# Performance work log

Hardware: AMD Instinct MI355X
Metric: run time of the kernel (lower is better)

Reference implementation:

```python
import jax, jax.numpy as jnp
import numpy as np

NUM_HEADS = 8
BN_EPS = 1e-3


def _conv2d(x, w, padding):
    # x: (B, Cin, H, W), w: (Cout, Cin, kh, kw)
    return jax.lax.conv_general_dilated(
        x, w, window_strides=(1, 1), padding=padding,
        dimension_numbers=("NCHW", "OIHW", "NCHW"))


def setup_inputs() -> dict:
    key = jax.random.key(0)
    ks = jax.random.split(key, 6)
    B, C, H, W = 8, 256, 64, 64
    L, D = 80, 256
    return {
        "img_feat": jax.random.normal(ks[0], (B, C, H, W), jnp.float32),
        "text_feats": jax.random.normal(ks[1], (B, L, D), jnp.float32),
        "proj_w": jax.random.normal(ks[2], (D, C, 1, 1), jnp.float32) * (1.0 / np.sqrt(C)),
        "proj_b": jax.random.normal(ks[3], (D,), jnp.float32) * 0.02,
        "attn_bias": jnp.zeros((NUM_HEADS,), jnp.float32),
        "scale": jnp.ones((1, NUM_HEADS, 1, 1), jnp.float32),
        "conv_w": jax.random.normal(ks[4], (C, C, 3, 3), jnp.float32) * (1.0 / np.sqrt(9 * C)),
        "bn_gamma": jnp.ones((C,), jnp.float32),
        "bn_beta": jnp.zeros((C,), jnp.float32),
        "bn_mean": jnp.zeros((C,), jnp.float32),
        "bn_var": jnp.ones((C,), jnp.float32),
    }


def reference(img_feat, text_feats, proj_w, proj_b, attn_bias, scale,
              conv_w, bn_gamma, bn_beta, bn_mean, bn_var):
    B, C, H, W = img_feat.shape
    hc = proj_w.shape[0] // NUM_HEADS  # head_channels

    # img_proj: 1x1 conv + bias -> (B, heads, hc, H, W)
    i_feat = _conv2d(img_feat, proj_w, "VALID") + proj_b[None, :, None, None]
    i_feat = i_feat.reshape(B, NUM_HEADS, hc, H, W)

    # text: (B, L, heads, hc)
    t_feat = text_feats.reshape(B, -1, NUM_HEADS, hc)

    # attn score over text tokens, then max over tokens
    attn = jnp.einsum("bmchw,bnmc->bmhwn", i_feat, t_feat)  # (B, heads, H, W, L)
    attn = jnp.max(attn, axis=-1)
    attn = attn / jnp.sqrt(jnp.asarray(hc, img_feat.dtype))
    attn = attn + attn_bias[None, :, None, None]
    attn = jax.nn.sigmoid(attn) * scale  # (B, heads, H, W)

    # project_conv: 3x3 conv (no bias) + BN (inference), no activation
    x = _conv2d(img_feat, conv_w, [(1, 1), (1, 1)])
    inv = bn_gamma / jnp.sqrt(bn_var + BN_EPS)
    x = x * inv[None, :, None, None] + (bn_beta - bn_mean * inv)[None, :, None, None]

    # gate per head and flatten back to (B, C, H, W)
    x = x.reshape(B, NUM_HEADS, -1, H, W) * attn[:, :, None]
    return x.reshape(B, -1, H, W)
```

## Files before the change

### kernel.cpp

```cpp
#include <hip/hip_runtime.h>
#include <cmath>

constexpr int kB  = 8;
constexpr int kC  = 256;
constexpr int kH  = 64;
constexpr int kW  = 64;
constexpr int kP  = kH * kW;
constexpr int kL  = 80;
constexpr int kD  = 256;
constexpr int kNH = 8;

typedef short  short8 __attribute__((ext_vector_type(8)));
typedef float  f32x4  __attribute__((ext_vector_type(4)));
typedef unsigned short ushort_t;

__device__ __forceinline__ ushort_t f2bf(float f) {
  unsigned u = __builtin_bit_cast(unsigned, f);
  u += 0x7fffu + ((u >> 16) & 1u);
  return (ushort_t)(u >> 16);
}

__device__ __forceinline__ short8 pack8(float4 a, float4 b) {
  ushort_t tmp[8] = {f2bf(a.x), f2bf(a.y), f2bf(a.z), f2bf(a.w),
                     f2bf(b.x), f2bf(b.y), f2bf(b.z), f2bf(b.w)};
  return *(short8*)tmp;
}

__global__ __launch_bounds__(256) void transpose_img_kernel(
    const float* __restrict__ img, ushort_t* __restrict__ imgT) {
  __shared__ float Ls[64 * 67];
  const int b   = blockIdx.x;
  const int p0  = blockIdx.y * 64;
  const int ci0 = blockIdx.z * 64;
  const int t   = threadIdx.x;

  for (int e = t; e < 4096; e += 256) {
    int ci = e >> 6, px = e & 63;
    Ls[px * 67 + ci] = img[((size_t)(b * kC + ci0 + ci)) * kP + p0 + px];
  }
  __syncthreads();
  for (int u = t; u < 512; u += 256) {
    int px = u >> 3, cq = (u & 7) * 8;
    ushort_t tmp[8];
#pragma unroll
    for (int j = 0; j < 8; j++) tmp[j] = f2bf(Ls[px * 67 + cq + j]);
    *(uint4*)&imgT[((size_t)(b * kP + p0 + px)) * kC + ci0 + cq] = *(uint4*)tmp;
  }
}

__global__ __launch_bounds__(256) void transpose_w2_kernel(
    const float* __restrict__ cw, ushort_t* __restrict__ w2) {
  int idx = blockIdx.x * 256 + threadIdx.x;
  if (idx >= 9 * kC * kC) return;
  int ci  = idx & 255;
  int co  = (idx >> 8) & 255;
  int tap = idx >> 16;
  w2[idx] = f2bf(cw[(co * kC + ci) * 9 + tap]);
}

__global__ __launch_bounds__(256) void attn_mfma_kernel(
    const ushort_t* __restrict__ imgT,
    const float* __restrict__ text,
    const float* __restrict__ pw,
    const float* __restrict__ pb,
    const float* __restrict__ bias,
    const float* __restrict__ scale,
    float* __restrict__ attn_out) {
  __shared__ ushort_t SI[64 * 264];

  const int b    = blockIdx.x;
  const int p0   = blockIdx.y * 64;
  const int t    = threadIdx.x;
  const int w    = t >> 6;
  const int lane = t & 63;
  const int lr   = lane & 15;
  const int lq   = lane >> 4;
  const int d0   = w * 64;

  const ushort_t* imgTb = imgT + (size_t)b * kP * kC;

  f32x4 acc[4][4] = {};

  for (int kc = 0; kc < kC; kc += 32) {
    short8 afr[4], bfr[4];
#pragma unroll
    for (int mt = 0; mt < 4; mt++) {
      const float* p = pw + (size_t)(d0 + mt * 16 + lr) * kC + kc + lq * 8;
      afr[mt] = pack8(*(const float4*)p, *(const float4*)(p + 4));
    }
#pragma unroll
    for (int nt = 0; nt < 4; nt++)
      bfr[nt] = *(const short8*)&imgTb[(size_t)(p0 + nt * 16 + lr) * kC + kc + lq * 8];
#pragma unroll
    for (int mt = 0; mt < 4; mt++)
#pragma unroll
      for (int nt = 0; nt < 4; nt++)
        acc[mt][nt] = __builtin_amdgcn_mfma_f32_16x16x32_bf16(afr[mt], bfr[nt], acc[mt][nt], 0, 0, 0);
  }

#pragma unroll
  for (int mt = 0; mt < 4; mt++) {
    float4 pb4 = *(const float4*)(pb + d0 + mt * 16 + lq * 4);
#pragma unroll
    for (int nt = 0; nt < 4; nt++) {
      ushort_t v[4];
      v[0] = f2bf(acc[mt][nt][0] + pb4.x);
      v[1] = f2bf(acc[mt][nt][1] + pb4.y);
      v[2] = f2bf(acc[mt][nt][2] + pb4.z);
      v[3] = f2bf(acc[mt][nt][3] + pb4.w);
      *(ulonglong1*)&SI[(nt * 16 + lr) * 264 + d0 + mt * 16 + lq * 4] = *(ulonglong1*)v;
    }
  }

  const float* textb = text + (size_t)b * kL * kD;
#pragma unroll
  for (int lh = 0; lh < 2; lh++) {
    const int h = 2 * w + lh;
    const float bh = bias[h], sh = scale[h];
    short8 atok[5];
#pragma unroll
    for (int mt = 0; mt < 5; mt++) {
      const float* p = textb + (size_t)(mt * 16 + lr) * kD + h * 32 + lq * 8;
      atok[mt] = pack8(*(const float4*)p, *(const float4*)(p + 4));
    }
#pragma unroll
    for (int nt = 0; nt < 4; nt++) {
      short8 bfr2 = *(const short8*)&SI[(nt * 16 + lr) * 264 + h * 32 + lq * 8];
      float vmax = -3.4e38f;
#pragma unroll
      for (int mt = 0; mt < 5; mt++) {
        f32x4 z = {};
        f32x4 d = __builtin_amdgcn_mfma_f32_16x16x32_bf16(atok[mt], bfr2, z, 0, 0, 0);
        vmax = fmaxf(vmax, fmaxf(fmaxf(d[0], d[1]), fmaxf(d[2], d[3])));
      }
      vmax = fmaxf(vmax, __shfl_xor(vmax, 16));
      vmax = fmaxf(vmax, __shfl_xor(vmax, 32));
      if (lq == 0) {
        float lg = vmax * 0.17677669529663687f + bh;
        float a  = sh / (1.0f + expf(-lg));
        attn_out[((size_t)(b * kNH + h)) * kP + p0 + nt * 16 + lr] = a;
      }
    }
  }
}

__global__ __launch_bounds__(256) void conv_mfma_kernel(
    const ushort_t* __restrict__ imgT,
    const ushort_t* __restrict__ w2,
    const float* __restrict__ gamma,
    const float* __restrict__ beta,
    const float* __restrict__ mean,
    const float* __restrict__ var,
    const float* __restrict__ attn,
    float* __restrict__ out) {
  __shared__ ushort_t Al[6 * 66 * 40];
  __shared__ ushort_t Wl[9 * 64 * 40];

  const int b   = blockIdx.x;
  const int h0  = blockIdx.y * 4;
  const int co0 = blockIdx.z * 64;
  const int t   = threadIdx.x;
  const int w   = t >> 6;
  const int lane = t & 63;
  const int lr  = lane & 15;
  const int lq  = lane >> 4;

  const ushort_t* imgTb = imgT + (size_t)b * kP * kC;

  f32x4 acc[4][4] = {};

  for (int kc = 0; kc < kC; kc += 32) {
    __syncthreads();
    for (int e = t; e < 6 * 66 * 4; e += 256) {
      int r   = e / 264;
      int rem = e - r * 264;
      int c   = rem >> 2;
      int cq  = (rem & 3) * 8;
      int row = h0 - 1 + r;
      uint4 v = make_uint4(0, 0, 0, 0);
      if (row >= 0 && row < kH && c >= 1 && c <= 64) {
        int px = row * kW + (c - 1);
        v = *(const uint4*)&imgTb[(size_t)px * kC + kc + cq];
      }
      *(uint4*)&Al[(r * 66 + c) * 40 + cq] = v;
    }
    {
      int e = t;
#pragma unroll
      for (int i = 0; i < 9; i++, e += 256) {
        int cq  = (e & 3) * 8;
        int co  = (e >> 2) & 63;
        int tap = e >> 8;
        uint4 v = *(const uint4*)&w2[((size_t)(tap * kC + co0 + co)) * kC + kc + cq];
        *(uint4*)&Wl[(tap * 64 + co) * 40 + cq] = v;
      }
    }
    __syncthreads();

    const int abase = (w * 66 + lr) * 40 + lq * 8;
    const int wbase = lr * 40 + lq * 8;
#pragma unroll
    for (int tap = 0; tap < 9; tap++) {
      const int kh = tap / 3, kw = tap % 3;
      short8 bi[4];
#pragma unroll
      for (int nt = 0; nt < 4; nt++)
        bi[nt] = *(const short8*)&Al[abase + (kh * 66 + kw + nt * 16) * 40];
      short8 aw[4];
#pragma unroll
      for (int mt = 0; mt < 4; mt++)
        aw[mt] = *(const short8*)&Wl[wbase + (tap * 64 + mt * 16) * 40];
#pragma unroll
      for (int mt = 0; mt < 4; mt++)
#pragma unroll
        for (int nt = 0; nt < 4; nt++)
          acc[mt][nt] = __builtin_amdgcn_mfma_f32_16x16x32_bf16(
              aw[mt], bi[nt], acc[mt][nt], 0, 0, 0);
    }
  }

  const int h = h0 + w;
  float* outb = out + (size_t)b * kC * kP + h * kW;
#pragma unroll
  for (int mt = 0; mt < 4; mt++) {
    const int head = (co0 + mt * 16) >> 5;
    const float* arow = attn + ((size_t)(b * kNH + head)) * kP + h * kW;
    float inv_v[4], bb_v[4];
#pragma unroll
    for (int reg = 0; reg < 4; reg++) {
      int co = co0 + mt * 16 + lq * 4 + reg;
      float inv = gamma[co] * rsqrtf(var[co] + 1e-3f);
      inv_v[reg] = inv;
      bb_v[reg]  = beta[co] - mean[co] * inv;
    }
#pragma unroll
    for (int nt = 0; nt < 4; nt++) {
      const int col = nt * 16 + lr;
      const float av = arow[col];
#pragma unroll
      for (int reg = 0; reg < 4; reg++) {
        int co = co0 + mt * 16 + lq * 4 + reg;
        outb[(size_t)co * kP + col] = (acc[mt][nt][reg] * inv_v[reg] + bb_v[reg]) * av;
      }
    }
  }
}

extern "C" void kernel_launch(void* const* d_in, const int* in_sizes, int n_in,
                              void* d_out, int out_size, void* d_ws, size_t ws_size,
                              hipStream_t stream) {
  const float* img   = (const float*)d_in[0];
  const float* text  = (const float*)d_in[1];
  const float* pw    = (const float*)d_in[2];
  const float* pb    = (const float*)d_in[3];
  const float* bias  = (const float*)d_in[4];
  const float* scale = (const float*)d_in[5];
  const float* cw    = (const float*)d_in[6];
  const float* gam   = (const float*)d_in[7];
  const float* bet   = (const float*)d_in[8];
  const float* mea   = (const float*)d_in[9];
  const float* va    = (const float*)d_in[10];
  float* out = (float*)d_out;

  char* ws = (char*)d_ws;
  float*    attn = (float*)ws;
  ushort_t* imgT = (ushort_t*)(ws + (1u << 20));
  ushort_t* w2   = (ushort_t*)(ws + (1u << 20) + (16u << 20));

  {
    dim3 grid(kB, kP / 64, kC / 64);
    transpose_img_kernel<<<grid, 256, 0, stream>>>(img, imgT);
  }
  transpose_w2_kernel<<<(9 * kC * kC + 255) / 256, 256, 0, stream>>>(cw, w2);

  {
    dim3 grid(kB, kP / 64);
    attn_mfma_kernel<<<grid, 256, 0, stream>>>(imgT, text, pw, pb, bias, scale, attn);
  }

  {
    dim3 grid(kB, kH / 4, kC / 64);
    conv_mfma_kernel<<<grid, 256, 0, stream>>>(imgT, w2, gam, bet, mea, va, attn, out);
  }
}
```

Measured before the change: 182.4 us.

## Load conv input fragments directly from global memory instead of LDS staging

The conv kernel no longer stages the image halo tile in shared memory. Each lane now reads its bf16 input fragments straight from global memory, with boundary clamping and zeroing at the edges, and skips rows that fall outside the image. The grid is reordered so the four output-channel blocks that share an input tile launch next to each other and can hit in cache, and a min-blocks-per-CU launch bound of 3 is added. This removes LDS footprint and one barrier-bound staging pass, but the MFMA inputs now depend on global/L2 latency with no explicit prefetch.

```diff
diff --git a/kernel.cpp b/kernel.cpp
--- a/kernel.cpp
+++ b/kernel.cpp
@@ -144,7 +144,7 @@
   }
 }
 
-__global__ __launch_bounds__(256) void conv_mfma_kernel(
+__global__ __launch_bounds__(256, 3) void conv_mfma_kernel(
     const ushort_t* __restrict__ imgT,
     const ushort_t* __restrict__ w2,
     const float* __restrict__ gamma,
@@ -153,37 +153,23 @@
     const float* __restrict__ var,
     const float* __restrict__ attn,
     float* __restrict__ out) {
-  __shared__ ushort_t Al[6 * 66 * 40];
   __shared__ ushort_t Wl[9 * 64 * 40];
 
-  const int b   = blockIdx.x;
-  const int h0  = blockIdx.y * 4;
-  const int co0 = blockIdx.z * 64;
+  const int co0 = blockIdx.x * 64;
+  const int b   = blockIdx.y;
+  const int h0  = blockIdx.z * 4;
   const int t   = threadIdx.x;
   const int w   = t >> 6;
   const int lane = t & 63;
   const int lr  = lane & 15;
   const int lq  = lane >> 4;
 
-  const ushort_t* imgTb = imgT + (size_t)b * kP * kC;
+  const ushort_t* imgTb = imgT + (size_t)b * kP * kC + lq * 8;
 
   f32x4 acc[4][4] = {};
 
   for (int kc = 0; kc < kC; kc += 32) {
     __syncthreads();
-    for (int e = t; e < 6 * 66 * 4; e += 256) {
-      int r   = e / 264;
-      int rem = e - r * 264;
-      int c   = rem >> 2;
-      int cq  = (rem & 3) * 8;
-      int row = h0 - 1 + r;
-      uint4 v = make_uint4(0, 0, 0, 0);
-      if (row >= 0 && row < kH && c >= 1 && c <= 64) {
-        int px = row * kW + (c - 1);
-        v = *(const uint4*)&imgTb[(size_t)px * kC + kc + cq];
-      }
-      *(uint4*)&Al[(r * 66 + c) * 40 + cq] = v;
-    }
     {
       int e = t;
 #pragma unroll
@@ -197,25 +183,44 @@
     }
     __syncthreads();
 
-    const int abase = (w * 66 + lr) * 40 + lq * 8;
     const int wbase = lr * 40 + lq * 8;
 #pragma unroll
-    for (int tap = 0; tap < 9; tap++) {
-      const int kh = tap / 3, kw = tap % 3;
-      short8 bi[4];
-#pragma unroll
-      for (int nt = 0; nt < 4; nt++)
-        bi[nt] = *(const short8*)&Al[abase + (kh * 66 + kw + nt * 16) * 40];
-      short8 aw[4];
-#pragma unroll
-      for (int mt = 0; mt < 4; mt++)
-        aw[mt] = *(const short8*)&Wl[wbase + (tap * 64 + mt * 16) * 40];
-#pragma unroll
-      for (int mt = 0; mt < 4; mt++)
-#pragma unroll
-        for (int nt = 0; nt < 4; nt++)
-          acc[mt][nt] = __builtin_amdgcn_mfma_f32_16x16x32_bf16(
-              aw[mt], bi[nt], acc[mt][nt], 0, 0, 0);
+    for (int kh = 0; kh < 3; kh++) {
+      const int r = h0 + w + kh - 1;
+      if (r < 0 || r >= kH) continue;
+      const ushort_t* rowp = imgTb + (size_t)(r * kW) * kC + kc;
+#pragma unroll
+      for (int kw = 0; kw < 3; kw++) {
+        const int tap = kh * 3 + kw;
+        short8 bi[4];
+#pragma unroll
+        for (int nt = 0; nt < 4; nt++) {
+          int col = nt * 16 + lr + kw - 1;
+          if (kw == 0 && nt == 0) {
+            int colc = col < 0 ? 0 : col;
+            short8 v = *(const short8*)(rowp + (size_t)colc * kC);
+            if (col < 0) v = (short8)0;
+            bi[nt] = v;
+          } else if (kw == 2 && nt == 3) {
+            int colc = col > 63 ? 63 : col;
+            short8 v = *(const short8*)(rowp + (size_t)colc * kC);
+            if (col > 63) v = (short8)0;
+            bi[nt] = v;
+          } else {
+            bi[nt] = *(const short8*)(rowp + (size_t)col * kC);
+          }
+        }
+        short8 aw[4];
+#pragma unroll
+        for (int mt = 0; mt < 4; mt++)
+          aw[mt] = *(const short8*)&Wl[wbase + (tap * 64 + mt * 16) * 40];
+#pragma unroll
+        for (int mt = 0; mt < 4; mt++)
+#pragma unroll
+          for (int nt = 0; nt < 4; nt++)
+            acc[mt][nt] = __builtin_amdgcn_mfma_f32_16x16x32_bf16(
+                aw[mt], bi[nt], acc[mt][nt], 0, 0, 0);
+      }
     }
   }
 
@@ -277,9 +282,8 @@
     dim3 grid(kB, kP / 64);
     attn_mfma_kernel<<<grid, 256, 0, stream>>>(imgT, text, pw, pb, bias, scale, attn);
   }
-
   {
-    dim3 grid(kB, kH / 4, kC / 64);
+    dim3 grid(kC / 64, kB, kH / 4);
     conv_mfma_kernel<<<grid, 256, 0, stream>>>(imgT, w2, gam, bet, mea, va, attn, out);
   }
 }
```

New measurement: 218.4 us. 1.2x slower.
